# Performance work log

Hardware: AMD Instinct MI355X
Metric: run time of the kernel (lower is better)

## Reference

```python
import jax, jax.numpy as jnp
import numpy as np

N, NU, R, NX, NY = 16384, 2, 256, 8, 2


def setup_inputs() -> dict:
    key = jax.random.key(0)
    ks = jax.random.split(key, 10)
    A = jax.random.normal(ks[0], (NX, NX), dtype=jnp.float32)
    # scale A to be stable (spectral radius < 1) so the 16k-step recurrence is well-behaved
    rho = jnp.max(jnp.abs(jnp.linalg.eigvals(A.astype(jnp.float32)))).real
    A = (A * (0.95 / rho)).astype(jnp.float32)
    return {
        "u": jax.random.normal(ks[1], (N, NU, R), dtype=jnp.float32),
        "x0": jax.random.normal(ks[2], (NX, R), dtype=jnp.float32),
        "A": A,
        "B_u": jax.random.normal(ks[3], (NX, NU), dtype=jnp.float32),
        "C_y": jax.random.normal(ks[4], (NY, NX), dtype=jnp.float32),
        "D_yu": jax.random.normal(ks[5], (NY, NU), dtype=jnp.float32),
        "u_mean": jax.random.normal(ks[6], (NU,), dtype=jnp.float32),
        "u_std": jax.random.uniform(ks[7], (NU,), dtype=jnp.float32, minval=0.5, maxval=1.5),
        "y_mean": jax.random.normal(ks[8], (NY,), dtype=jnp.float32),
        "y_std": jax.random.uniform(ks[9], (NY,), dtype=jnp.float32, minval=0.5, maxval=1.5),
    }


def reference(u, x0, A, B_u, C_y, D_yu, u_mean, u_std, y_mean, y_std):
    # normalize input as in _simulate_core
    un = (u - u_mean.reshape(1, -1, 1)) / u_std.reshape(1, -1, 1)  # (N, nu, R)

    def step(x, uk):
        # x: (nx, R), uk: (nu, R)
        y = C_y @ x + D_yu @ uk      # (ny, R)
        x_next = A @ x + B_u @ uk    # (nx, R)
        return x_next, (y, x)

    _, (Y, X) = jax.lax.scan(step, x0, un)  # Y: (N, ny, R), X: (N, nx, R)

    # denormalize output
    y = Y * y_std.reshape(1, -1, 1) + y_mean.reshape(1, -1, 1)
    return y, X
```

## Files before the change

kernel.cpp:

```cpp
#include <hip/hip_runtime.h>


#define NSTEPS 16384
#define NUI 2
#define RB 256
#define NXS 8
#define NYO 2
#define LF 32
#define NC1 (NSTEPS / LF)
#define NSUP 8
#define NC2B (NC1 / NSUP)

__global__ __launch_bounds__(RB) void phase1_k(
    const float* __restrict__ u, const float* __restrict__ A,
    const float* __restrict__ Bu, const float* __restrict__ um,
    const float* __restrict__ us, float* __restrict__ d32) {
    const int c = blockIdx.x;
    const int r = threadIdx.x;
    float a[NXS][NXS];
    #pragma unroll
    for (int i = 0; i < NXS; ++i)
        #pragma unroll
        for (int j = 0; j < NXS; ++j) a[i][j] = A[i * NXS + j];
    float b0[NXS], b1[NXS];
    #pragma unroll
    for (int i = 0; i < NXS; ++i) { b0[i] = Bu[i * NUI]; b1[i] = Bu[i * NUI + 1]; }
    const float um0 = um[0], um1 = um[1];
    const float is0 = 1.0f / us[0], is1 = 1.0f / us[1];
    float t[NXS];
    #pragma unroll
    for (int i = 0; i < NXS; ++i) t[i] = 0.f;
    const float* up = u + (size_t)c * LF * NUI * RB + r;
    #pragma unroll 4
    for (int j = 0; j < LF; ++j) {
        const float u0 = (up[0]  - um0) * is0;
        const float u1 = (up[RB] - um1) * is1;
        up += NUI * RB;
        float nt[NXS];
        #pragma unroll
        for (int i = 0; i < NXS; ++i) {
            float acc = fmaf(b0[i], u0, b1[i] * u1);
            #pragma unroll
            for (int k = 0; k < NXS; ++k) acc = fmaf(a[i][k], t[k], acc);
            nt[i] = acc;
        }
        #pragma unroll
        for (int i = 0; i < NXS; ++i) t[i] = nt[i];
    }
    float* dp = d32 + (size_t)c * NXS * RB + r;
    #pragma unroll
    for (int i = 0; i < NXS; ++i) dp[i * RB] = t[i];
}

__global__ __launch_bounds__(RB) void combine8_k(
    const float* __restrict__ d32, const float* __restrict__ A,
    float* __restrict__ d256) {
    __shared__ float Ms[64];
    __shared__ float A32s[64];
    const int m = blockIdx.x;
    const int t = threadIdx.x;
    const int r = t;

    float xq[NSUP][NXS];
    #pragma unroll
    for (int q = 0; q < NSUP; ++q) {
        const float* dq = d32 + (size_t)(NSUP * m + q) * NXS * RB + r;
        #pragma unroll
        for (int i = 0; i < NXS; ++i) xq[q][i] = dq[i * RB];
    }

    if (t < 64) Ms[t] = A[t];
    __syncthreads();
    {
        const int pi = t >> 3, pj = t & 7;
        for (int it = 0; it < 5; ++it) {
            float acc = 0.f;
            if (t < 64) {
                #pragma unroll
                for (int k = 0; k < 8; ++k) acc += Ms[pi * 8 + k] * Ms[k * 8 + pj];
            }
            __syncthreads();
            if (t < 64) Ms[t] = acc;
            __syncthreads();
        }
        if (t < 64) A32s[t] = Ms[t];
        __syncthreads();
    }

    float a32[NXS][NXS];
    #pragma unroll
    for (int i = 0; i < NXS; ++i)
        #pragma unroll
        for (int j = 0; j < NXS; ++j) a32[i][j] = A32s[i * 8 + j];

    float s[NXS];
    #pragma unroll
    for (int i = 0; i < NXS; ++i) s[i] = xq[0][i];
    #pragma unroll
    for (int q = 1; q < NSUP; ++q) {
        float nt[NXS];
        #pragma unroll
        for (int i = 0; i < NXS; ++i) {
            float acc = xq[q][i];
            #pragma unroll
            for (int k = 0; k < NXS; ++k) acc = fmaf(a32[i][k], s[k], acc);
            nt[i] = acc;
        }
        #pragma unroll
        for (int i = 0; i < NXS; ++i) s[i] = nt[i];
    }
    float* o = d256 + (size_t)m * NXS * RB + r;
    #pragma unroll
    for (int i = 0; i < NXS; ++i) o[i * RB] = s[i];
}

__global__ __launch_bounds__(64) void phase2_k(
    const float* __restrict__ x0, const float* __restrict__ A,
    const float* __restrict__ d256, float* __restrict__ s256) {
    __shared__ float Ms[64];
    const int t = threadIdx.x;
    const int r = blockIdx.x * 64 + t;

    float s[NXS];
    #pragma unroll
    for (int i = 0; i < NXS; ++i) s[i] = x0[i * RB + r];
    float P[8][NXS];
    #pragma unroll
    for (int sl = 0; sl < 8; ++sl) {
        const float* dp = d256 + (size_t)sl * NXS * RB + r;
        #pragma unroll
        for (int i = 0; i < NXS; ++i) P[sl][i] = dp[i * RB];
    }

    Ms[t] = A[t];
    __syncthreads();
    {
        const int pi = t >> 3, pj = t & 7;
        for (int it = 0; it < 8; ++it) {
            float acc = 0.f;
            #pragma unroll
            for (int k = 0; k < 8; ++k) acc += Ms[pi * 8 + k] * Ms[k * 8 + pj];
            __syncthreads();
            Ms[t] = acc;
            __syncthreads();
        }
    }
    float m[NXS][NXS];
    #pragma unroll
    for (int i = 0; i < NXS; ++i)
        #pragma unroll
        for (int j = 0; j < NXS; ++j) m[i][j] = Ms[i * 8 + j];

    for (int c = 0; c < NC2B; c += 8) {
        #pragma unroll
        for (int sl = 0; sl < 8; ++sl) {
            const int cc = c + sl;
            float* sp = s256 + (size_t)cc * NXS * RB + r;
            #pragma unroll
            for (int i = 0; i < NXS; ++i) sp[i * RB] = s[i];
            float ns[NXS];
            #pragma unroll
            for (int i = 0; i < NXS; ++i) {
                float acc = P[sl][i];
                #pragma unroll
                for (int k = 0; k < NXS; ++k) acc = fmaf(m[i][k], s[k], acc);
                ns[i] = acc;
            }
            if (cc + 8 < NC2B) {
                const float* dp = d256 + (size_t)(cc + 8) * NXS * RB + r;
                #pragma unroll
                for (int i = 0; i < NXS; ++i) P[sl][i] = dp[i * RB];
            }
            #pragma unroll
            for (int i = 0; i < NXS; ++i) s[i] = ns[i];
        }
    }
}

__global__ __launch_bounds__(RB) void phase3_k(
    const float* __restrict__ u, const float* __restrict__ s256,
    const float* __restrict__ d32, const float* __restrict__ A,
    const float* __restrict__ Bu, const float* __restrict__ Cy,
    const float* __restrict__ Dyu, const float* __restrict__ um,
    const float* __restrict__ us, const float* __restrict__ ym,
    const float* __restrict__ ys, float* __restrict__ Y,
    float* __restrict__ X) {
    __shared__ float Ms[64];
    __shared__ float A32s[64];
    const int c = blockIdx.x;
    const int t = threadIdx.x;
    const int r = t;
    const int m = c >> 3;
    const int p = c & 7;

    float tv[NXS];
    {
        const float* sp = s256 + (size_t)m * NXS * RB + r;
        #pragma unroll
        for (int i = 0; i < NXS; ++i) tv[i] = sp[i * RB];
    }

    if (t < 64) Ms[t] = A[t];
    __syncthreads();
    {
        const int pi = t >> 3, pj = t & 7;
        for (int it = 0; it < 5; ++it) {
            float acc = 0.f;
            if (t < 64) {
                #pragma unroll
                for (int k = 0; k < 8; ++k) acc += Ms[pi * 8 + k] * Ms[k * 8 + pj];
            }
            __syncthreads();
            if (t < 64) Ms[t] = acc;
            __syncthreads();
        }
        if (t < 64) A32s[t] = Ms[t];
        __syncthreads();
    }

    if (p) {
        float a32[NXS][NXS];
        #pragma unroll
        for (int i = 0; i < NXS; ++i)
            #pragma unroll
            for (int j = 0; j < NXS; ++j) a32[i][j] = A32s[i * 8 + j];
        float Pa[NXS], Pb[NXS];
        const float* dp0 = d32 + (size_t)(NSUP * m) * NXS * RB + r;
        #pragma unroll
        for (int i = 0; i < NXS; ++i) Pa[i] = dp0[i * RB];
        #pragma unroll
        for (int q = 0; q < NSUP - 1; ++q) {
            if (q < p) {
                if (q + 1 < p) {
                    const float* dn = d32 + (size_t)(NSUP * m + q + 1) * NXS * RB + r;
                    if (q & 1) {
                        #pragma unroll
                        for (int i = 0; i < NXS; ++i) Pa[i] = dn[i * RB];
                    } else {
                        #pragma unroll
                        for (int i = 0; i < NXS; ++i) Pb[i] = dn[i * RB];
                    }
                }
                float nt[NXS];
                #pragma unroll
                for (int i = 0; i < NXS; ++i) {
                    float acc = (q & 1) ? Pb[i] : Pa[i];
                    #pragma unroll
                    for (int k = 0; k < NXS; ++k) acc = fmaf(a32[i][k], tv[k], acc);
                    nt[i] = acc;
                }
                #pragma unroll
                for (int i = 0; i < NXS; ++i) tv[i] = nt[i];
            }
        }
    }

    float a[NXS][NXS];
    #pragma unroll
    for (int i = 0; i < NXS; ++i)
        #pragma unroll
        for (int j = 0; j < NXS; ++j) a[i][j] = A[i * NXS + j];
    float b0[NXS], b1[NXS], c0[NXS], c1[NXS];
    #pragma unroll
    for (int i = 0; i < NXS; ++i) { b0[i] = Bu[i * NUI]; b1[i] = Bu[i * NUI + 1]; }
    #pragma unroll
    for (int k = 0; k < NXS; ++k) { c0[k] = Cy[k]; c1[k] = Cy[NXS + k]; }
    const float d00 = Dyu[0], d01 = Dyu[1], d10 = Dyu[2], d11 = Dyu[3];
    const float um0 = um[0], um1 = um[1];
    const float is0 = 1.0f / us[0], is1 = 1.0f / us[1];
    const float ym0 = ym[0], ym1 = ym[1], ys0 = ys[0], ys1 = ys[1];

    const float* up = u + (size_t)c * LF * NUI * RB + r;
    float* Xp = X + (size_t)c * LF * NXS * RB + r;
    float* Yp = Y + (size_t)c * LF * NYO * RB + r;
    #pragma unroll 4
    for (int j = 0; j < LF; ++j) {
        const float u0 = (up[0]  - um0) * is0;
        const float u1 = (up[RB] - um1) * is1;
        up += NUI * RB;
        #pragma unroll
        for (int i = 0; i < NXS; ++i)
            __builtin_nontemporal_store(tv[i], Xp + i * RB);
        Xp += NXS * RB;
        float y0 = fmaf(d00, u0, d01 * u1);
        float y1 = fmaf(d10, u0, d11 * u1);
        #pragma unroll
        for (int k = 0; k < NXS; ++k) {
            y0 = fmaf(c0[k], tv[k], y0);
            y1 = fmaf(c1[k], tv[k], y1);
        }
        __builtin_nontemporal_store(fmaf(y0, ys0, ym0), Yp);
        __builtin_nontemporal_store(fmaf(y1, ys1, ym1), Yp + RB);
        Yp += NYO * RB;
        float nt[NXS];
        #pragma unroll
        for (int i = 0; i < NXS; ++i) {
            float acc = fmaf(b0[i], u0, b1[i] * u1);
            #pragma unroll
            for (int k = 0; k < NXS; ++k) acc = fmaf(a[i][k], tv[k], acc);
            nt[i] = acc;
        }
        #pragma unroll
        for (int i = 0; i < NXS; ++i) tv[i] = nt[i];
    }
}

extern "C" void kernel_launch(void* const* d_in, const int* in_sizes, int n_in,
                              void* d_out, int out_size, void* d_ws, size_t ws_size,
                              hipStream_t stream) {
    const float* u   = (const float*)d_in[0];
    const float* x0  = (const float*)d_in[1];
    const float* A   = (const float*)d_in[2];
    const float* Bu  = (const float*)d_in[3];
    const float* Cy  = (const float*)d_in[4];
    const float* Dyu = (const float*)d_in[5];
    const float* um  = (const float*)d_in[6];
    const float* us  = (const float*)d_in[7];
    const float* ym  = (const float*)d_in[8];
    const float* ys  = (const float*)d_in[9];

    float* Y = (float*)d_out;
    float* X = Y + (size_t)NSTEPS * NYO * RB;

    float* ws   = (float*)d_ws;
    float* d32  = ws;
    float* d256 = d32 + (size_t)NC1 * NXS * RB;
    float* s256 = d256 + (size_t)NC2B * NXS * RB;

    phase1_k<<<NC1, RB, 0, stream>>>(u, A, Bu, um, us, d32);
    combine8_k<<<NC2B, RB, 0, stream>>>(d32, A, d256);
    phase2_k<<<4, 64, 0, stream>>>(x0, A, d256, s256);
    phase3_k<<<NC1, RB, 0, stream>>>(u, s256, d32, A, Bu, Cy, Dyu,
                                     um, us, ym, ys, Y, X);
}
```

Measured before the change: 236.6 us.

## Fuse four scan phases into one kernel synchronized by global atomic flags

Replaces the four-kernel chunked scan (local chunk, combine, serial prefix, replay) with a single persistent-style kernel. Blocks publish chunk summaries and coordinate through agent-scope atomic counters, so the last block in each group of eight computes the group summary and its prefix. The normalized inputs are kept in shared memory so the replay pass does not reread u from global memory. This removes three kernel launches and the serial phase2 bottleneck, but it relies on all 512 blocks being co-resident to avoid deadlock, and it adds a memset plus spin-wait latency.

```diff
diff --git a/kernel.cpp b/kernel.cpp
--- a/kernel.cpp
+++ b/kernel.cpp
@@ -10,13 +10,42 @@
 #define NC1 (NSTEPS / LF)
 #define NSUP 8
 #define NC2B (NC1 / NSUP)
-
-__global__ __launch_bounds__(RB) void phase1_k(
-    const float* __restrict__ u, const float* __restrict__ A,
-    const float* __restrict__ Bu, const float* __restrict__ um,
-    const float* __restrict__ us, float* __restrict__ d32) {
+#define CNT_TGT (7u * RB)
+#define DCNT_TGT ((unsigned)NC2B * RB)
+#define FS_TGT ((unsigned)RB)
+
+__device__ __forceinline__ void waitflag(unsigned int* f, unsigned int tgt) {
+    if (threadIdx.x == 0) {
+        while (__hip_atomic_load(f, __ATOMIC_RELAXED, __HIP_MEMORY_SCOPE_AGENT) < tgt)
+            __builtin_amdgcn_s_sleep(2);
+        (void)__hip_atomic_load(f, __ATOMIC_ACQUIRE, __HIP_MEMORY_SCOPE_AGENT);
+    }
+    __syncthreads();
+}
+
+__global__ __launch_bounds__(RB, 2) void fused_k(
+    const float* __restrict__ u, const float* __restrict__ x0,
+    const float* __restrict__ A, const float* __restrict__ Bu,
+    const float* __restrict__ Cy, const float* __restrict__ Dyu,
+    const float* __restrict__ um, const float* __restrict__ us,
+    const float* __restrict__ ym, const float* __restrict__ ys,
+    float* __restrict__ Y, float* __restrict__ X,
+    float* __restrict__ d32, float* __restrict__ d256,
+    float* __restrict__ s256, unsigned int* __restrict__ flags) {
+    __shared__ float uL[LF][NUI][RB];
+    __shared__ float Ms[64];
+    __shared__ float A32s[64];
+    __shared__ float A256s[64];
+
     const int c = blockIdx.x;
-    const int r = threadIdx.x;
+    const int t = threadIdx.x;
+    const int r = t;
+    const int m = c >> 3;
+    const int p = c & 7;
+    unsigned int* cnt  = flags;
+    unsigned int* dcnt = flags + NC2B;
+    unsigned int* fs   = flags + NC2B + 1;
+
     float a[NXS][NXS];
     #pragma unroll
     for (int i = 0; i < NXS; ++i)
@@ -27,195 +56,165 @@
     for (int i = 0; i < NXS; ++i) { b0[i] = Bu[i * NUI]; b1[i] = Bu[i * NUI + 1]; }
     const float um0 = um[0], um1 = um[1];
     const float is0 = 1.0f / us[0], is1 = 1.0f / us[1];
-    float t[NXS];
+    float tv[NXS];
     #pragma unroll
-    for (int i = 0; i < NXS; ++i) t[i] = 0.f;
-    const float* up = u + (size_t)c * LF * NUI * RB + r;
-    #pragma unroll 4
-    for (int j = 0; j < LF; ++j) {
-        const float u0 = (up[0]  - um0) * is0;
-        const float u1 = (up[RB] - um1) * is1;
-        up += NUI * RB;
-        float nt[NXS];
-        #pragma unroll
-        for (int i = 0; i < NXS; ++i) {
-            float acc = fmaf(b0[i], u0, b1[i] * u1);
-            #pragma unroll
-            for (int k = 0; k < NXS; ++k) acc = fmaf(a[i][k], t[k], acc);
-            nt[i] = acc;
-        }
-        #pragma unroll
-        for (int i = 0; i < NXS; ++i) t[i] = nt[i];
-    }
-    float* dp = d32 + (size_t)c * NXS * RB + r;
-    #pragma unroll
-    for (int i = 0; i < NXS; ++i) dp[i * RB] = t[i];
-}
-
-__global__ __launch_bounds__(RB) void combine8_k(
-    const float* __restrict__ d32, const float* __restrict__ A,
-    float* __restrict__ d256) {
-    __shared__ float Ms[64];
-    __shared__ float A32s[64];
-    const int m = blockIdx.x;
-    const int t = threadIdx.x;
-    const int r = t;
-
-    float xq[NSUP][NXS];
-    #pragma unroll
-    for (int q = 0; q < NSUP; ++q) {
-        const float* dq = d32 + (size_t)(NSUP * m + q) * NXS * RB + r;
-        #pragma unroll
-        for (int i = 0; i < NXS; ++i) xq[q][i] = dq[i * RB];
+    for (int i = 0; i < NXS; ++i) tv[i] = 0.f;
+    {
+        const float* up = u + (size_t)c * LF * NUI * RB + r;
+        #pragma unroll 4
+        for (int j = 0; j < LF; ++j) {
+            const float u0 = (up[0]  - um0) * is0;
+            const float u1 = (up[RB] - um1) * is1;
+            up += NUI * RB;
+            uL[j][0][r] = u0;
+            uL[j][1][r] = u1;
+            float nt[NXS];
+            #pragma unroll
+            for (int i = 0; i < NXS; ++i) {
+                float acc = fmaf(b0[i], u0, b1[i] * u1);
+                #pragma unroll
+                for (int k = 0; k < NXS; ++k) acc = fmaf(a[i][k], tv[k], acc);
+                nt[i] = acc;
+            }
+            #pragma unroll
+            for (int i = 0; i < NXS; ++i) tv[i] = nt[i];
+        }
+    }
+    if (p != 7) {
+        float* dp = d32 + (size_t)c * NXS * RB + r;
+        #pragma unroll
+        for (int i = 0; i < NXS; ++i) dp[i * RB] = tv[i];
+        __hip_atomic_fetch_add(&cnt[m], 1u, __ATOMIC_RELEASE,
+                               __HIP_MEMORY_SCOPE_AGENT);
     }
 
     if (t < 64) Ms[t] = A[t];
     __syncthreads();
     {
         const int pi = t >> 3, pj = t & 7;
-        for (int it = 0; it < 5; ++it) {
+        #pragma unroll
+        for (int it = 0; it < 8; ++it) {
             float acc = 0.f;
             if (t < 64) {
                 #pragma unroll
                 for (int k = 0; k < 8; ++k) acc += Ms[pi * 8 + k] * Ms[k * 8 + pj];
             }
             __syncthreads();
-            if (t < 64) Ms[t] = acc;
+            if (t < 64) {
+                Ms[t] = acc;
+                if (it == 4) A32s[t] = acc;
+            }
             __syncthreads();
         }
-        if (t < 64) A32s[t] = Ms[t];
+        if (t < 64) A256s[t] = Ms[t];
         __syncthreads();
     }
 
-    float a32[NXS][NXS];
-    #pragma unroll
-    for (int i = 0; i < NXS; ++i)
-        #pragma unroll
-        for (int j = 0; j < NXS; ++j) a32[i][j] = A32s[i * 8 + j];
-
-    float s[NXS];
-    #pragma unroll
-    for (int i = 0; i < NXS; ++i) s[i] = xq[0][i];
-    #pragma unroll
-    for (int q = 1; q < NSUP; ++q) {
-        float nt[NXS];
-        #pragma unroll
-        for (int i = 0; i < NXS; ++i) {
-            float acc = xq[q][i];
-            #pragma unroll
-            for (int k = 0; k < NXS; ++k) acc = fmaf(a32[i][k], s[k], acc);
-            nt[i] = acc;
-        }
-        #pragma unroll
-        for (int i = 0; i < NXS; ++i) s[i] = nt[i];
-    }
-    float* o = d256 + (size_t)m * NXS * RB + r;
-    #pragma unroll
-    for (int i = 0; i < NXS; ++i) o[i * RB] = s[i];
-}
-
-__global__ __launch_bounds__(64) void phase2_k(
-    const float* __restrict__ x0, const float* __restrict__ A,
-    const float* __restrict__ d256, float* __restrict__ s256) {
-    __shared__ float Ms[64];
-    const int t = threadIdx.x;
-    const int r = blockIdx.x * 64 + t;
-
-    float s[NXS];
-    #pragma unroll
-    for (int i = 0; i < NXS; ++i) s[i] = x0[i * RB + r];
-    float P[8][NXS];
-    #pragma unroll
-    for (int sl = 0; sl < 8; ++sl) {
-        const float* dp = d256 + (size_t)sl * NXS * RB + r;
-        #pragma unroll
-        for (int i = 0; i < NXS; ++i) P[sl][i] = dp[i * RB];
-    }
-
-    Ms[t] = A[t];
-    __syncthreads();
-    {
-        const int pi = t >> 3, pj = t & 7;
-        for (int it = 0; it < 8; ++it) {
-            float acc = 0.f;
-            #pragma unroll
-            for (int k = 0; k < 8; ++k) acc += Ms[pi * 8 + k] * Ms[k * 8 + pj];
-            __syncthreads();
-            Ms[t] = acc;
-            __syncthreads();
-        }
-    }
-    float m[NXS][NXS];
-    #pragma unroll
-    for (int i = 0; i < NXS; ++i)
-        #pragma unroll
-        for (int j = 0; j < NXS; ++j) m[i][j] = Ms[i * 8 + j];
-
-    for (int c = 0; c < NC2B; c += 8) {
-        #pragma unroll
-        for (int sl = 0; sl < 8; ++sl) {
-            const int cc = c + sl;
-            float* sp = s256 + (size_t)cc * NXS * RB + r;
-            #pragma unroll
-            for (int i = 0; i < NXS; ++i) sp[i * RB] = s[i];
-            float ns[NXS];
-            #pragma unroll
-            for (int i = 0; i < NXS; ++i) {
-                float acc = P[sl][i];
-                #pragma unroll
-                for (int k = 0; k < NXS; ++k) acc = fmaf(m[i][k], s[k], acc);
-                ns[i] = acc;
-            }
-            if (cc + 8 < NC2B) {
-                const float* dp = d256 + (size_t)(cc + 8) * NXS * RB + r;
-                #pragma unroll
-                for (int i = 0; i < NXS; ++i) P[sl][i] = dp[i * RB];
-            }
-            #pragma unroll
-            for (int i = 0; i < NXS; ++i) s[i] = ns[i];
-        }
-    }
-}
-
-__global__ __launch_bounds__(RB) void phase3_k(
-    const float* __restrict__ u, const float* __restrict__ s256,
-    const float* __restrict__ d32, const float* __restrict__ A,
-    const float* __restrict__ Bu, const float* __restrict__ Cy,
-    const float* __restrict__ Dyu, const float* __restrict__ um,
-    const float* __restrict__ us, const float* __restrict__ ym,
-    const float* __restrict__ ys, float* __restrict__ Y,
-    float* __restrict__ X) {
-    __shared__ float Ms[64];
-    __shared__ float A32s[64];
-    const int c = blockIdx.x;
-    const int t = threadIdx.x;
-    const int r = t;
-    const int m = c >> 3;
-    const int p = c & 7;
-
-    float tv[NXS];
-    {
+    float sb[NXS];
+
+    if (p == 7) {
+        float xv[NXS];
+        #pragma unroll
+        for (int i = 0; i < NXS; ++i) xv[i] = x0[i * RB + r];
+
+        waitflag(&cnt[m], CNT_TGT);
+        {
+            float a32[NXS][NXS];
+            #pragma unroll
+            for (int i = 0; i < NXS; ++i)
+                #pragma unroll
+                for (int j = 0; j < NXS; ++j) a32[i][j] = A32s[i * 8 + j];
+            float xq[NSUP - 1][NXS];
+            #pragma unroll
+            for (int q = 0; q < NSUP - 1; ++q) {
+                const float* dq = d32 + (size_t)(NSUP * m + q) * NXS * RB + r;
+                #pragma unroll
+                for (int i = 0; i < NXS; ++i) xq[q][i] = dq[i * RB];
+            }
+            float s[NXS];
+            #pragma unroll
+            for (int i = 0; i < NXS; ++i) s[i] = xq[0][i];
+            #pragma unroll
+            for (int q = 1; q < NSUP - 1; ++q) {
+                float nt[NXS];
+                #pragma unroll
+                for (int i = 0; i < NXS; ++i) {
+                    float acc = xq[q][i];
+                    #pragma unroll
+                    for (int k = 0; k < NXS; ++k) acc = fmaf(a32[i][k], s[k], acc);
+                    nt[i] = acc;
+                }
+                #pragma unroll
+                for (int i = 0; i < NXS; ++i) s[i] = nt[i];
+            }
+            {
+                float nt[NXS];
+                #pragma unroll
+                for (int i = 0; i < NXS; ++i) {
+                    float acc = tv[i];
+                    #pragma unroll
+                    for (int k = 0; k < NXS; ++k) acc = fmaf(a32[i][k], s[k], acc);
+                    nt[i] = acc;
+                }
+                #pragma unroll
+                for (int i = 0; i < NXS; ++i) s[i] = nt[i];
+            }
+            float* o = d256 + (size_t)m * NXS * RB + r;
+            #pragma unroll
+            for (int i = 0; i < NXS; ++i) o[i * RB] = s[i];
+        }
+        __hip_atomic_fetch_add(dcnt, 1u, __ATOMIC_RELEASE,
+                               __HIP_MEMORY_SCOPE_AGENT);
+
+        #pragma unroll
+        for (int i = 0; i < NXS; ++i) sb[i] = xv[i];
+        if (m > 0) {
+            waitflag(dcnt, DCNT_TGT);
+            float a256[NXS][NXS];
+            #pragma unroll
+            for (int i = 0; i < NXS; ++i)
+                #pragma unroll
+                for (int j = 0; j < NXS; ++j) a256[i][j] = A256s[i * 8 + j];
+            for (int base = 0; base < m; base += 8) {
+                float T[8][NXS];
+                #pragma unroll
+                for (int k = 0; k < 8; ++k) {
+                    if (base + k < m) {
+                        const float* dq = d256 + (size_t)(base + k) * NXS * RB + r;
+                        #pragma unroll
+                        for (int i = 0; i < NXS; ++i) T[k][i] = dq[i * RB];
+                    }
+                }
+                #pragma unroll
+                for (int k = 0; k < 8; ++k) {
+                    if (base + k < m) {
+                        float nt[NXS];
+                        #pragma unroll
+                        for (int i = 0; i < NXS; ++i) {
+                            float acc = T[k][i];
+                            #pragma unroll
+                            for (int kk = 0; kk < NXS; ++kk)
+                                acc = fmaf(a256[i][kk], sb[kk], acc);
+                            nt[i] = acc;
+                        }
+                        #pragma unroll
+                        for (int i = 0; i < NXS; ++i) sb[i] = nt[i];
+                    }
+                }
+            }
+        }
+        {
+            float* sp = s256 + (size_t)m * NXS * RB + r;
+            #pragma unroll
+            for (int i = 0; i < NXS; ++i) sp[i * RB] = sb[i];
+        }
+        __hip_atomic_fetch_add(&fs[m], 1u, __ATOMIC_RELEASE,
+                               __HIP_MEMORY_SCOPE_AGENT);
+    } else {
+        waitflag(&fs[m], FS_TGT);
         const float* sp = s256 + (size_t)m * NXS * RB + r;
         #pragma unroll
-        for (int i = 0; i < NXS; ++i) tv[i] = sp[i * RB];
-    }
-
-    if (t < 64) Ms[t] = A[t];
-    __syncthreads();
-    {
-        const int pi = t >> 3, pj = t & 7;
-        for (int it = 0; it < 5; ++it) {
-            float acc = 0.f;
-            if (t < 64) {
-                #pragma unroll
-                for (int k = 0; k < 8; ++k) acc += Ms[pi * 8 + k] * Ms[k * 8 + pj];
-            }
-            __syncthreads();
-            if (t < 64) Ms[t] = acc;
-            __syncthreads();
-        }
-        if (t < 64) A32s[t] = Ms[t];
-        __syncthreads();
+        for (int i = 0; i < NXS; ++i) sb[i] = sp[i * RB];
     }
 
     if (p) {
@@ -224,70 +223,53 @@
         for (int i = 0; i < NXS; ++i)
             #pragma unroll
             for (int j = 0; j < NXS; ++j) a32[i][j] = A32s[i * 8 + j];
-        float Pa[NXS], Pb[NXS];
-        const float* dp0 = d32 + (size_t)(NSUP * m) * NXS * RB + r;
-        #pragma unroll
-        for (int i = 0; i < NXS; ++i) Pa[i] = dp0[i * RB];
+        float P[NSUP - 1][NXS];
         #pragma unroll
         for (int q = 0; q < NSUP - 1; ++q) {
             if (q < p) {
-                if (q + 1 < p) {
-                    const float* dn = d32 + (size_t)(NSUP * m + q + 1) * NXS * RB + r;
-                    if (q & 1) {
-                        #pragma unroll
-                        for (int i = 0; i < NXS; ++i) Pa[i] = dn[i * RB];
-                    } else {
-                        #pragma unroll
-                        for (int i = 0; i < NXS; ++i) Pb[i] = dn[i * RB];
-                    }
-                }
+                const float* dq = d32 + (size_t)(NSUP * m + q) * NXS * RB + r;
+                #pragma unroll
+                for (int i = 0; i < NXS; ++i) P[q][i] = dq[i * RB];
+            }
+        }
+        #pragma unroll
+        for (int q = 0; q < NSUP - 1; ++q) {
+            if (q < p) {
                 float nt[NXS];
                 #pragma unroll
                 for (int i = 0; i < NXS; ++i) {
-                    float acc = (q & 1) ? Pb[i] : Pa[i];
+                    float acc = P[q][i];
                     #pragma unroll
-                    for (int k = 0; k < NXS; ++k) acc = fmaf(a32[i][k], tv[k], acc);
+                    for (int k = 0; k < NXS; ++k) acc = fmaf(a32[i][k], sb[k], acc);
                     nt[i] = acc;
                 }
                 #pragma unroll
-                for (int i = 0; i < NXS; ++i) tv[i] = nt[i];
-            }
-        }
-    }
-
-    float a[NXS][NXS];
-    #pragma unroll
-    for (int i = 0; i < NXS; ++i)
-        #pragma unroll
-        for (int j = 0; j < NXS; ++j) a[i][j] = A[i * NXS + j];
-    float b0[NXS], b1[NXS], c0[NXS], c1[NXS];
-    #pragma unroll
-    for (int i = 0; i < NXS; ++i) { b0[i] = Bu[i * NUI]; b1[i] = Bu[i * NUI + 1]; }
+                for (int i = 0; i < NXS; ++i) sb[i] = nt[i];
+            }
+        }
+    }
+
+    float c0[NXS], c1[NXS];
     #pragma unroll
     for (int k = 0; k < NXS; ++k) { c0[k] = Cy[k]; c1[k] = Cy[NXS + k]; }
     const float d00 = Dyu[0], d01 = Dyu[1], d10 = Dyu[2], d11 = Dyu[3];
-    const float um0 = um[0], um1 = um[1];
-    const float is0 = 1.0f / us[0], is1 = 1.0f / us[1];
     const float ym0 = ym[0], ym1 = ym[1], ys0 = ys[0], ys1 = ys[1];
-
-    const float* up = u + (size_t)c * LF * NUI * RB + r;
     float* Xp = X + (size_t)c * LF * NXS * RB + r;
     float* Yp = Y + (size_t)c * LF * NYO * RB + r;
     #pragma unroll 4
     for (int j = 0; j < LF; ++j) {
-        const float u0 = (up[0]  - um0) * is0;
-        const float u1 = (up[RB] - um1) * is1;
-        up += NUI * RB;
+        const float u0 = uL[j][0][r];
+        const float u1 = uL[j][1][r];
         #pragma unroll
         for (int i = 0; i < NXS; ++i)
-            __builtin_nontemporal_store(tv[i], Xp + i * RB);
+            __builtin_nontemporal_store(sb[i], Xp + i * RB);
         Xp += NXS * RB;
         float y0 = fmaf(d00, u0, d01 * u1);
         float y1 = fmaf(d10, u0, d11 * u1);
         #pragma unroll
         for (int k = 0; k < NXS; ++k) {
-            y0 = fmaf(c0[k], tv[k], y0);
-            y1 = fmaf(c1[k], tv[k], y1);
+            y0 = fmaf(c0[k], sb[k], y0);
+            y1 = fmaf(c1[k], sb[k], y1);
         }
         __builtin_nontemporal_store(fmaf(y0, ys0, ym0), Yp);
         __builtin_nontemporal_store(fmaf(y1, ys1, ym1), Yp + RB);
@@ -297,11 +279,11 @@
         for (int i = 0; i < NXS; ++i) {
             float acc = fmaf(b0[i], u0, b1[i] * u1);
             #pragma unroll
-            for (int k = 0; k < NXS; ++k) acc = fmaf(a[i][k], tv[k], acc);
+            for (int k = 0; k < NXS; ++k) acc = fmaf(a[i][k], sb[k], acc);
             nt[i] = acc;
         }
         #pragma unroll
-        for (int i = 0; i < NXS; ++i) tv[i] = nt[i];
+        for (int i = 0; i < NXS; ++i) sb[i] = nt[i];
     }
 }
 
@@ -326,10 +308,9 @@
     float* d32  = ws;
     float* d256 = d32 + (size_t)NC1 * NXS * RB;
     float* s256 = d256 + (size_t)NC2B * NXS * RB;
-
-    phase1_k<<<NC1, RB, 0, stream>>>(u, A, Bu, um, us, d32);
-    combine8_k<<<NC2B, RB, 0, stream>>>(d32, A, d256);
-    phase2_k<<<4, 64, 0, stream>>>(x0, A, d256, s256);
-    phase3_k<<<NC1, RB, 0, stream>>>(u, s256, d32, A, Bu, Cy, Dyu,
-                                     um, us, ym, ys, Y, X);
+    unsigned int* flags = (unsigned int*)(s256 + (size_t)NC2B * NXS * RB);
+
+    hipMemsetAsync(flags, 0, 1024, stream);
+    fused_k<<<NC1, RB, 0, stream>>>(u, x0, A, Bu, Cy, Dyu, um, us, ym, ys,
+                                    Y, X, d32, d256, s256, flags);
 }
```

Result: slower. 393.7 us (+66.4%).

## Fuse serial phase-2 scan into phase-3 via redundant per-block prefix recomputation

Applied to the files above, without the earlier changes.

Removes the separate low-parallelism phase-2 kernel and the s256 workspace. Each phase-3 block now computes its own starting state by applying A^256 across all preceding d256 partial sums from x0, then A^32 for the intra-super-chunk offsets. The d32 loads are also batched up front instead of being double-buffered. This trades a kernel launch and a serialized tiny grid for redundant work that is imbalanced across blocks, since later blocks iterate up to 63 steps.

```diff
diff --git a/kernel.cpp b/kernel.cpp
--- a/kernel.cpp
+++ b/kernel.cpp
@@ -114,108 +114,81 @@
     for (int i = 0; i < NXS; ++i) o[i * RB] = s[i];
 }
 
-__global__ __launch_bounds__(64) void phase2_k(
-    const float* __restrict__ x0, const float* __restrict__ A,
-    const float* __restrict__ d256, float* __restrict__ s256) {
+__global__ __launch_bounds__(RB) void phase3_k(
+    const float* __restrict__ u, const float* __restrict__ x0,
+    const float* __restrict__ d32, const float* __restrict__ d256,
+    const float* __restrict__ A, const float* __restrict__ Bu,
+    const float* __restrict__ Cy, const float* __restrict__ Dyu,
+    const float* __restrict__ um, const float* __restrict__ us,
+    const float* __restrict__ ym, const float* __restrict__ ys,
+    float* __restrict__ Y, float* __restrict__ X) {
     __shared__ float Ms[64];
+    __shared__ float A32s[64];
+    __shared__ float A256s[64];
+    const int c = blockIdx.x;
     const int t = threadIdx.x;
-    const int r = blockIdx.x * 64 + t;
-
-    float s[NXS];
-    #pragma unroll
-    for (int i = 0; i < NXS; ++i) s[i] = x0[i * RB + r];
-    float P[8][NXS];
-    #pragma unroll
-    for (int sl = 0; sl < 8; ++sl) {
-        const float* dp = d256 + (size_t)sl * NXS * RB + r;
-        #pragma unroll
-        for (int i = 0; i < NXS; ++i) P[sl][i] = dp[i * RB];
-    }
-
-    Ms[t] = A[t];
+    const int r = t;
+    const int m = c >> 3;
+    const int p = c & 7;
+
+    float sb[NXS];
+    #pragma unroll
+    for (int i = 0; i < NXS; ++i) sb[i] = x0[i * RB + r];
+
+    if (t < 64) Ms[t] = A[t];
     __syncthreads();
     {
         const int pi = t >> 3, pj = t & 7;
         for (int it = 0; it < 8; ++it) {
             float acc = 0.f;
-            #pragma unroll
-            for (int k = 0; k < 8; ++k) acc += Ms[pi * 8 + k] * Ms[k * 8 + pj];
+            if (t < 64) {
+                #pragma unroll
+                for (int k = 0; k < 8; ++k) acc += Ms[pi * 8 + k] * Ms[k * 8 + pj];
+            }
             __syncthreads();
-            Ms[t] = acc;
+            if (t < 64) {
+                Ms[t] = acc;
+                if (it == 4) A32s[t] = acc;
+            }
             __syncthreads();
         }
-    }
-    float m[NXS][NXS];
-    #pragma unroll
-    for (int i = 0; i < NXS; ++i)
-        #pragma unroll
-        for (int j = 0; j < NXS; ++j) m[i][j] = Ms[i * 8 + j];
-
-    for (int c = 0; c < NC2B; c += 8) {
-        #pragma unroll
-        for (int sl = 0; sl < 8; ++sl) {
-            const int cc = c + sl;
-            float* sp = s256 + (size_t)cc * NXS * RB + r;
-            #pragma unroll
-            for (int i = 0; i < NXS; ++i) sp[i * RB] = s[i];
-            float ns[NXS];
-            #pragma unroll
-            for (int i = 0; i < NXS; ++i) {
-                float acc = P[sl][i];
-                #pragma unroll
-                for (int k = 0; k < NXS; ++k) acc = fmaf(m[i][k], s[k], acc);
-                ns[i] = acc;
-            }
-            if (cc + 8 < NC2B) {
-                const float* dp = d256 + (size_t)(cc + 8) * NXS * RB + r;
-                #pragma unroll
-                for (int i = 0; i < NXS; ++i) P[sl][i] = dp[i * RB];
-            }
-            #pragma unroll
-            for (int i = 0; i < NXS; ++i) s[i] = ns[i];
-        }
-    }
-}
-
-__global__ __launch_bounds__(RB) void phase3_k(
-    const float* __restrict__ u, const float* __restrict__ s256,
-    const float* __restrict__ d32, const float* __restrict__ A,
-    const float* __restrict__ Bu, const float* __restrict__ Cy,
-    const float* __restrict__ Dyu, const float* __restrict__ um,
-    const float* __restrict__ us, const float* __restrict__ ym,
-    const float* __restrict__ ys, float* __restrict__ Y,
-    float* __restrict__ X) {
-    __shared__ float Ms[64];
-    __shared__ float A32s[64];
-    const int c = blockIdx.x;
-    const int t = threadIdx.x;
-    const int r = t;
-    const int m = c >> 3;
-    const int p = c & 7;
-
-    float tv[NXS];
-    {
-        const float* sp = s256 + (size_t)m * NXS * RB + r;
-        #pragma unroll
-        for (int i = 0; i < NXS; ++i) tv[i] = sp[i * RB];
-    }
-
-    if (t < 64) Ms[t] = A[t];
-    __syncthreads();
-    {
-        const int pi = t >> 3, pj = t & 7;
-        for (int it = 0; it < 5; ++it) {
-            float acc = 0.f;
-            if (t < 64) {
-                #pragma unroll
-                for (int k = 0; k < 8; ++k) acc += Ms[pi * 8 + k] * Ms[k * 8 + pj];
-            }
-            __syncthreads();
-            if (t < 64) Ms[t] = acc;
-            __syncthreads();
-        }
-        if (t < 64) A32s[t] = Ms[t];
+        if (t < 64) A256s[t] = Ms[t];
         __syncthreads();
+    }
+
+    if (m > 0) {
+        float a256[NXS][NXS];
+        #pragma unroll
+        for (int i = 0; i < NXS; ++i)
+            #pragma unroll
+            for (int j = 0; j < NXS; ++j) a256[i][j] = A256s[i * 8 + j];
+        for (int base = 0; base < m; base += 8) {
+            float T[8][NXS];
+            #pragma unroll
+            for (int k = 0; k < 8; ++k) {
+                if (base + k < m) {
+                    const float* dq = d256 + (size_t)(base + k) * NXS * RB + r;
+                    #pragma unroll
+                    for (int i = 0; i < NXS; ++i) T[k][i] = dq[i * RB];
+                }
+            }
+            #pragma unroll
+            for (int k = 0; k < 8; ++k) {
+                if (base + k < m) {
+                    float nt[NXS];
+                    #pragma unroll
+                    for (int i = 0; i < NXS; ++i) {
+                        float acc = T[k][i];
+                        #pragma unroll
+                        for (int kk = 0; kk < NXS; ++kk)
+                            acc = fmaf(a256[i][kk], sb[kk], acc);
+                        nt[i] = acc;
+                    }
+                    #pragma unroll
+                    for (int i = 0; i < NXS; ++i) sb[i] = nt[i];
+                }
+            }
+        }
     }
 
     if (p) {
@@ -224,33 +197,28 @@
         for (int i = 0; i < NXS; ++i)
             #pragma unroll
             for (int j = 0; j < NXS; ++j) a32[i][j] = A32s[i * 8 + j];
-        float Pa[NXS], Pb[NXS];
-        const float* dp0 = d32 + (size_t)(NSUP * m) * NXS * RB + r;
-        #pragma unroll
-        for (int i = 0; i < NXS; ++i) Pa[i] = dp0[i * RB];
+        float P[NSUP - 1][NXS];
         #pragma unroll
         for (int q = 0; q < NSUP - 1; ++q) {
             if (q < p) {
-                if (q + 1 < p) {
-                    const float* dn = d32 + (size_t)(NSUP * m + q + 1) * NXS * RB + r;
-                    if (q & 1) {
-                        #pragma unroll
-                        for (int i = 0; i < NXS; ++i) Pa[i] = dn[i * RB];
-                    } else {
-                        #pragma unroll
-                        for (int i = 0; i < NXS; ++i) Pb[i] = dn[i * RB];
-                    }
-                }
+                const float* dq = d32 + (size_t)(NSUP * m + q) * NXS * RB + r;
+                #pragma unroll
+                for (int i = 0; i < NXS; ++i) P[q][i] = dq[i * RB];
+            }
+        }
+        #pragma unroll
+        for (int q = 0; q < NSUP - 1; ++q) {
+            if (q < p) {
                 float nt[NXS];
                 #pragma unroll
                 for (int i = 0; i < NXS; ++i) {
-                    float acc = (q & 1) ? Pb[i] : Pa[i];
+                    float acc = P[q][i];
                     #pragma unroll
-                    for (int k = 0; k < NXS; ++k) acc = fmaf(a32[i][k], tv[k], acc);
+                    for (int k = 0; k < NXS; ++k) acc = fmaf(a32[i][k], sb[k], acc);
                     nt[i] = acc;
                 }
                 #pragma unroll
-                for (int i = 0; i < NXS; ++i) tv[i] = nt[i];
+                for (int i = 0; i < NXS; ++i) sb[i] = nt[i];
             }
         }
     }
@@ -280,14 +248,14 @@
         up += NUI * RB;
         #pragma unroll
         for (int i = 0; i < NXS; ++i)
-            __builtin_nontemporal_store(tv[i], Xp + i * RB);
+            __builtin_nontemporal_store(sb[i], Xp + i * RB);
         Xp += NXS * RB;
         float y0 = fmaf(d00, u0, d01 * u1);
         float y1 = fmaf(d10, u0, d11 * u1);
         #pragma unroll
         for (int k = 0; k < NXS; ++k) {
-            y0 = fmaf(c0[k], tv[k], y0);
-            y1 = fmaf(c1[k], tv[k], y1);
+            y0 = fmaf(c0[k], sb[k], y0);
+            y1 = fmaf(c1[k], sb[k], y1);
         }
         __builtin_nontemporal_store(fmaf(y0, ys0, ym0), Yp);
         __builtin_nontemporal_store(fmaf(y1, ys1, ym1), Yp + RB);
@@ -297,11 +265,11 @@
         for (int i = 0; i < NXS; ++i) {
             float acc = fmaf(b0[i], u0, b1[i] * u1);
             #pragma unroll
-            for (int k = 0; k < NXS; ++k) acc = fmaf(a[i][k], tv[k], acc);
+            for (int k = 0; k < NXS; ++k) acc = fmaf(a[i][k], sb[k], acc);
             nt[i] = acc;
         }
         #pragma unroll
-        for (int i = 0; i < NXS; ++i) tv[i] = nt[i];
+        for (int i = 0; i < NXS; ++i) sb[i] = nt[i];
     }
 }
 
@@ -325,11 +293,9 @@
     float* ws   = (float*)d_ws;
     float* d32  = ws;
     float* d256 = d32 + (size_t)NC1 * NXS * RB;
-    float* s256 = d256 + (size_t)NC2B * NXS * RB;
 
     phase1_k<<<NC1, RB, 0, stream>>>(u, A, Bu, um, us, d32);
     combine8_k<<<NC2B, RB, 0, stream>>>(d32, A, d256);
-    phase2_k<<<4, 64, 0, stream>>>(x0, A, d256, s256);
-    phase3_k<<<NC1, RB, 0, stream>>>(u, s256, d32, A, Bu, Cy, Dyu,
+    phase3_k<<<NC1, RB, 0, stream>>>(u, x0, d32, d256, A, Bu, Cy, Dyu,
                                      um, us, ym, ys, Y, X);
 }
```

After: 223.6 us. 5.5% less time.
